# Kernel tuning notes

Measured on AMD Instinct MI355X. Metric: run time of the kernel, lower is better.

The kernel has to match this reference:

```python
import jax, jax.numpy as jnp
import numpy as np

B, T, I, H, L = 32768, 30, 4, 64, 32


def _lstm_layer(x, Wih, Whh, bih, bhh):
    """PyTorch-semantics single-layer LSTM, batch_first. Returns (outputs [B,T,H], h_T [B,H])."""
    # Precompute input contribution for all timesteps: [B, T, 4H]
    xg = jnp.einsum('bti,gi->btg', x, Wih) + bih + bhh
    Hh = Whh.shape[1]
    h0 = jnp.zeros((x.shape[0], Hh), x.dtype)

    def step(carry, xg_t):
        h, c = carry
        g = xg_t + h @ Whh.T  # [B, 4H]
        i, f, gg, o = jnp.split(g, 4, axis=-1)  # PyTorch gate order i,f,g,o
        c = jax.nn.sigmoid(f) * c + jax.nn.sigmoid(i) * jnp.tanh(gg)
        h = jax.nn.sigmoid(o) * jnp.tanh(c)
        return (h, c), h

    (hT, _), hs = jax.lax.scan(step, (h0, h0), jnp.swapaxes(xg, 0, 1))
    return jnp.swapaxes(hs, 0, 1), hT


def setup_inputs() -> dict:
    key = jax.random.key(0)
    ks = jax.random.split(key, 20)
    s = 0.1  # weight scale for numerical stability
    inp = {
        'x': jax.random.normal(ks[0], (B, T, I), jnp.float32),
        'enc1_Wih': s * jax.random.normal(ks[1], (4 * H, I), jnp.float32),
        'enc1_Whh': s * jax.random.normal(ks[2], (4 * H, H), jnp.float32),
        'enc1_bih': s * jax.random.normal(ks[3], (4 * H,), jnp.float32),
        'enc1_bhh': s * jax.random.normal(ks[4], (4 * H,), jnp.float32),
        'enc2_Wih': s * jax.random.normal(ks[5], (4 * L, H), jnp.float32),
        'enc2_Whh': s * jax.random.normal(ks[6], (4 * L, L), jnp.float32),
        'enc2_bih': s * jax.random.normal(ks[7], (4 * L,), jnp.float32),
        'enc2_bhh': s * jax.random.normal(ks[8], (4 * L,), jnp.float32),
        'dec1_Wih': s * jax.random.normal(ks[9], (4 * H, L), jnp.float32),
        'dec1_Whh': s * jax.random.normal(ks[10], (4 * H, H), jnp.float32),
        'dec1_bih': s * jax.random.normal(ks[11], (4 * H,), jnp.float32),
        'dec1_bhh': s * jax.random.normal(ks[12], (4 * H,), jnp.float32),
        'dec2_Wih': s * jax.random.normal(ks[13], (4 * I, H), jnp.float32),
        'dec2_Whh': s * jax.random.normal(ks[14], (4 * I, I), jnp.float32),
        'dec2_bih': s * jax.random.normal(ks[15], (4 * I,), jnp.float32),
        'dec2_bhh': s * jax.random.normal(ks[16], (4 * I,), jnp.float32),
    }
    return inp


def reference(x, enc1_Wih, enc1_Whh, enc1_bih, enc1_bhh,
              enc2_Wih, enc2_Whh, enc2_bih, enc2_bhh,
              dec1_Wih, dec1_Whh, dec1_bih, dec1_bhh,
              dec2_Wih, dec2_Whh, dec2_bih, dec2_bhh):
    seq_len = x.shape[1]
    out, _ = _lstm_layer(x, enc1_Wih, enc1_Whh, enc1_bih, enc1_bhh)
    out, h = _lstm_layer(out, enc2_Wih, enc2_Whh, enc2_bih, enc2_bhh)
    latent = jnp.repeat(h[:, None, :], seq_len, axis=1)  # [B, T, L]
    out, _ = _lstm_layer(latent, dec1_Wih, dec1_Whh, dec1_bih, dec1_bhh)
    out, _ = _lstm_layer(out, dec2_Wih, dec2_Whh, dec2_bih, dec2_bhh)
    return out
```

## Files before the change

### kernel.cpp

```cpp
#include <hip/hip_runtime.h>
#include <stdint.h>


typedef unsigned short u16;
typedef unsigned int u32;
typedef __attribute__((ext_vector_type(8))) short bf16x8;
typedef __attribute__((ext_vector_type(4))) float f32x4;
typedef __attribute__((ext_vector_type(16))) float f32x16;
typedef __attribute__((ext_vector_type(4))) u32 u32x4;
typedef __attribute__((ext_vector_type(2))) u32 u32x2;

#define BATCH 32768
#define TT 30
#define IN 4
#define WAVES 12
#define BLOCKT (WAVES * 64)
#define MBC 32
#define NCL 4
#define BPB (NCL * MBC)

#define LOG2E 1.4426950408889634f
#define LOG2E2 2.8853900817779268f

#define O_WHH1 0
#define O_FOLD 8192
#define O_WIH2 10240
#define O_WHH2 14336
#define O_WHH3 0
#define O_WIH3 8192
#define O_WIH4 12288
#define O_W4HHF 12800
#define O_B2F 16384
#define O_B3F 16512
#define O_B4F 16768
#define O_BUFS 16784
#define PBUF 1664
#define SMEM_WORDS (O_BUFS + NCL * PBUF)
#define SMEM_BYTES (SMEM_WORDS * 4)

#define WB() __builtin_amdgcn_wave_barrier()
#define MFMA32(a, b, c) __builtin_amdgcn_mfma_f32_32x32x16_bf16((a), (b), (c), 0, 0, 0)
#define MFMA16(a, b, c) __builtin_amdgcn_mfma_f32_16x16x32_bf16((a), (b), (c), 0, 0, 0)

__device__ __forceinline__ u16 f2bf(float f) {
    u32 u = __float_as_uint(f);
    u += 0x7fffu + ((u >> 16) & 1u);
    return (u16)(u >> 16);
}
__device__ __forceinline__ float bf2f(u16 v) { return __uint_as_float(((u32)v) << 16); }

__device__ __forceinline__ u32 cvtpk2(float a, float b) {
    u32 d;
    asm("v_cvt_pk_bf16_f32 %0, %1, %2" : "=v"(d) : "v"(a), "v"(b));
    return d;
}

__device__ __forceinline__ float unitH(float yi, float yf, float yg, float yo, float& c) {
    const float ei = __builtin_amdgcn_exp2f(-yi);
    const float ef = __builtin_amdgcn_exp2f(-yf);
    const float eg = __builtin_amdgcn_exp2f(yg);
    const float eo = __builtin_amdgcn_exp2f(-yo);
    const float Z = (1.f + ei) * (1.f + eg);
    const float X = 1.f + ef;
    const float num = fmaf(eg - 1.f, X, c * Z);
    c = num * __builtin_amdgcn_rcpf(X * Z);
    const float ec = __builtin_amdgcn_exp2f(c * LOG2E2);
    return (ec - 1.f) * __builtin_amdgcn_rcpf((1.f + eo) * (1.f + ec));
}

template <int KT16, int GS>
__device__ __forceinline__ void stage32(u16* dst, const float* src, int N, int tid) {
    const int K = KT16 * 16;
    const int total = N * K;
    for (int idx = tid; idx < total; idx += BLOCKT) {
        const int j = idx & 7;
        const int l = (idx >> 3) & 63;
        const int pr = idx >> 9;
        const int kt = pr % KT16;
        const int nt = pr / KT16;
        const int n = nt * 32 + (l & 31);
        const int k = kt * 16 + ((l >> 5) << 3) + j;
        const float s = (((n >> GS) & 3) == 2) ? LOG2E2 : LOG2E;
        dst[idx] = f2bf(src[n * K + k] * s);
    }
}

template <int KT, int GS>
__device__ __forceinline__ void stage16(u16* dst, const float* src, int N, int tid) {
    const int K = KT * 32;
    const int total = N * K;
    for (int idx = tid; idx < total; idx += BLOCKT) {
        const int j = idx & 7;
        const int l = (idx >> 3) & 63;
        const int pr = idx >> 9;
        const int kt = pr & (KT - 1);
        const int nt = pr / KT;
        const int n = (nt << 4) | (l & 15);
        const int k = (kt << 5) + ((l >> 4) << 3) + j;
        const float s = (((n >> GS) & 3) == 2) ? LOG2E2 : LOG2E;
        dst[idx] = f2bf(src[n * K + k] * s);
    }
}

#define LD8(P, IDX) (*reinterpret_cast<const bf16x8*>((P) + ((IDX) * 64 + lane) * 8))

#define BINIT(DST, BP, RB)                                                               \
    _Pragma("unroll") for (int p_ = 0; p_ < 4; ++p_) {                                   \
        const f32x4 b_ = *reinterpret_cast<const f32x4*>((BP) + (RB) + p_ * 8 + 4 * hi); \
        (DST)[4 * p_ + 0] = b_[0]; (DST)[4 * p_ + 1] = b_[1];                            \
        (DST)[4 * p_ + 2] = b_[2]; (DST)[4 * p_ + 3] = b_[3];                            \
    }

#define CELL16(AI, AF, AG, AO, CST, IMG, BKT)                                                        \
    _Pragma("unroll") for (int p_ = 0; p_ < 4; ++p_) {                                               \
        const float h0_ = unitH((AI)[4*p_+0], (AF)[4*p_+0], (AG)[4*p_+0], (AO)[4*p_+0], (CST)[4*p_+0]); \
        const float h1_ = unitH((AI)[4*p_+1], (AF)[4*p_+1], (AG)[4*p_+1], (AO)[4*p_+1], (CST)[4*p_+1]); \
        const float h2_ = unitH((AI)[4*p_+2], (AF)[4*p_+2], (AG)[4*p_+2], (AO)[4*p_+2], (CST)[4*p_+2]); \
        const float h3_ = unitH((AI)[4*p_+3], (AF)[4*p_+3], (AG)[4*p_+3], (AO)[4*p_+3], (CST)[4*p_+3]); \
        u32x2 wv_;                                                                                   \
        wv_.x = cvtpk2(h0_, h1_);                                                                    \
        wv_.y = cvtpk2(h2_, h3_);                                                                    \
        *reinterpret_cast<u32x2*>((IMG) + (((BKT) + (p_ >> 1)) * 64 + (p_ & 1) * 32 + c31) * 8 + 4 * hi) = wv_; \
    }

#define E1G(DST, G) {                                                  \
        f32x16 a_ = MFMA32(foldr[G], xB, z16);                         \
        a_ = MFMA32(LD8(Whh1p, (2 * (G) + role) * 4 + 0), h1B0, a_);   \
        a_ = MFMA32(LD8(Whh1p, (2 * (G) + role) * 4 + 1), h1B1, a_);   \
        a_ = MFMA32(LD8(Whh1p, (2 * (G) + role) * 4 + 2), h1B2, a_);   \
        a_ = MFMA32(LD8(Whh1p, (2 * (G) + role) * 4 + 3), h1B3, a_);   \
        DST = a_; }

#define E2G(DST, G) {                                                  \
        f32x16 a_; BINIT(a_, b2f, (G) * 32)                            \
        a_ = MFMA32(LD8(Wih2p, (G) * 4 + 0), h1B0, a_);                \
        a_ = MFMA32(LD8(Wih2p, (G) * 4 + 1), h1B1, a_);                \
        a_ = MFMA32(LD8(Wih2p, (G) * 4 + 2), h1B2, a_);                \
        a_ = MFMA32(LD8(Wih2p, (G) * 4 + 3), h1B3, a_);                \
        a_ = MFMA32(LD8(Whh2p, (G) * 2 + 0), h2B0, a_);                \
        a_ = MFMA32(LD8(Whh2p, (G) * 2 + 1), h2B1, a_);                \
        DST = a_; }

#define D1G(DST, G) {                                                  \
        f32x16 a_; BINIT(a_, b3f, (2 * (G) + role) * 32)               \
        a_ = MFMA32(LD8(Wih3p, (2 * (G) + role) * 2 + 0), latB0, a_);  \
        a_ = MFMA32(LD8(Wih3p, (2 * (G) + role) * 2 + 1), latB1, a_);  \
        a_ = MFMA32(LD8(Whh3p, (2 * (G) + role) * 4 + 0), h3B0, a_);   \
        a_ = MFMA32(LD8(Whh3p, (2 * (G) + role) * 4 + 1), h3B1, a_);   \
        a_ = MFMA32(LD8(Whh3p, (2 * (G) + role) * 4 + 2), h3B2, a_);   \
        a_ = MFMA32(LD8(Whh3p, (2 * (G) + role) * 4 + 3), h3B3, a_);   \
        DST = a_; }
#define D1G0(DST, G) {                                                 \
        f32x16 a_; BINIT(a_, b3f, (2 * (G) + role) * 32)               \
        a_ = MFMA32(LD8(Wih3p, (2 * (G) + role) * 2 + 0), latB0, a_);  \
        a_ = MFMA32(LD8(Wih3p, (2 * (G) + role) * 2 + 1), latB1, a_);  \
        DST = a_; }

#define D2ADDR(M, BH) ((((2 * (M) + (quad >> 1)) * 64) + (quad & 1) * 32 + (BH) * 16 + col16) * 8)

#define DEC2BODY(T) {                                                                   \
        f32x4 a0 = b4v, a1 = b4v;                                                       \
        _Pragma("unroll") for (int r_ = 0; r_ < 4; ++r_) {                              \
            float s0 = a0[r_], s1 = a1[r_];                                             \
            s0 = fmaf(w4r[r_].x, hv0.x, s0); s0 = fmaf(w4r[r_].y, hv0.y, s0);           \
            s0 = fmaf(w4r[r_].z, hv0.z, s0); s0 = fmaf(w4r[r_].w, hv0.w, s0);           \
            s1 = fmaf(w4r[r_].x, hv1.x, s1); s1 = fmaf(w4r[r_].y, hv1.y, s1);           \
            s1 = fmaf(w4r[r_].z, hv1.z, s1); s1 = fmaf(w4r[r_].w, hv1.w, s1);           \
            a0[r_] = s0; a1[r_] = s1;                                                   \
        }                                                                               \
        a0 = MFMA16(w4a0, dB00, a0); a0 = MFMA16(w4a1, dB10, a0);                       \
        a1 = MFMA16(w4a0, dB01, a1); a1 = MFMA16(w4a1, dB11, a1);                       \
        WB();                                                                           \
        *reinterpret_cast<f32x4*>(gbuf + col16 * 16 + quad * 4) = a0;                   \
        *reinterpret_cast<f32x4*>(gbuf + (16 + col16) * 16 + quad * 4) = a1;            \
        WB();                                                                           \
        {                                                                               \
            const int u4_ = lane & 3, mb_ = lane >> 2;                                  \
            const float h0_ = unitH(gbuf[mb_ * 16 + u4_], gbuf[mb_ * 16 + 4 + u4_],     \
                                    gbuf[mb_ * 16 + 8 + u4_], gbuf[mb_ * 16 + 12 + u4_], c4a); \
            out[((size_t)(b0w + mb_) * TT + (T)) * IN + u4_] = h0_;                     \
            bufH4[mb_ * 4 + u4_] = h0_;                                                 \
            const int b1_ = 16 + mb_;                                                   \
            const float h1_ = unitH(gbuf[b1_ * 16 + u4_], gbuf[b1_ * 16 + 4 + u4_],     \
                                    gbuf[b1_ * 16 + 8 + u4_], gbuf[b1_ * 16 + 12 + u4_], c4b); \
            out[((size_t)(b0w + b1_) * TT + (T)) * IN + u4_] = h1_;                     \
            bufH4[b1_ * 4 + u4_] = h1_;                                                 \
        }                                                                               \
        WB(); }

__global__ __launch_bounds__(BLOCKT)
void lstm_ae(
    const float* __restrict__ x,
    const float* __restrict__ w1ih, const float* __restrict__ w1hh,
    const float* __restrict__ b1i, const float* __restrict__ b1h,
    const float* __restrict__ w2ih, const float* __restrict__ w2hh,
    const float* __restrict__ b2i, const float* __restrict__ b2h,
    const float* __restrict__ w3ih, const float* __restrict__ w3hh,
    const float* __restrict__ b3i, const float* __restrict__ b3h,
    const float* __restrict__ w4ih, const float* __restrict__ w4hh,
    const float* __restrict__ b4i, const float* __restrict__ b4h,
    float* __restrict__ out) {
    extern __shared__ float smem[];
    float* W = smem;

    const int tid = threadIdx.x;
    const int wave = tid >> 6, lane = tid & 63;
    const int cl = wave / 3, role = wave % 3;
    const int c31 = lane & 31, hi = lane >> 5;
    const int col16 = lane & 15, quad = lane >> 4;

    float* pb = smem + O_BUFS + cl * PBUF;
    u16* h1img = (u16*)pb;
    u16* h2img = (u16*)(pb + 1024);
    float* gbuf = pb + 1024;
    float* bufH4 = pb + 1536;

    const int b0w = blockIdx.x * BPB + cl * MBC;

    stage32<4, 6>((u16*)(W + O_WHH1), w1hh, 256, tid);
    stage32<4, 5>((u16*)(W + O_WIH2), w2ih, 128, tid);
    stage32<2, 5>((u16*)(W + O_WHH2), w2hh, 128, tid);
    {
        u16* F = (u16*)(W + O_FOLD);
        for (int idx = tid; idx < 4096; idx += BLOCKT) {
            const int j = idx & 7;
            const int l = (idx >> 3) & 63;
            const int nt = idx >> 9;
            const int m = nt * 32 + (l & 31);
            const int hif = l >> 5;
            const float sc = ((m >> 6) == 2) ? LOG2E2 : LOG2E;
            u16 v = 0;
            if (!hif) {
                v = f2bf(w1ih[m * 4 + (j & 3)] * sc);
            } else if (j < 4) {
                const float w = w1ih[m * 4 + j] * sc;
                v = f2bf(w - bf2f(f2bf(w)));
            } else if (j == 4) {
                v = f2bf((b1i[m] + b1h[m]) * sc);
            } else if (j == 5) {
                const float b = (b1i[m] + b1h[m]) * sc;
                v = f2bf(b - bf2f(f2bf(b)));
            }
            F[idx] = v;
        }
    }
    float* b2f = W + O_B2F;
    float* b3f = W + O_B3F;
    float* b4f = W + O_B4F;
    for (int i = tid; i < 128; i += BLOCKT)
        b2f[i] = (b2i[i] + b2h[i]) * (((i >> 5) == 2) ? LOG2E2 : LOG2E);
    for (int i = tid; i < 256; i += BLOCKT)
        b3f[i] = (b3i[i] + b3h[i]) * (((i >> 6) == 2) ? LOG2E2 : LOG2E);
    for (int i = tid; i < 16; i += BLOCKT)
        b4f[i] = (b4i[i] + b4h[i]) * (((i >> 2) == 2) ? LOG2E2 : LOG2E);
    if (role == 2) {
        u32* z = (u32*)h2img;
        for (int i = lane; i < 512; i += 64) z[i] = 0u;
    }
    __syncthreads();

    const u16* Whh1p = (const u16*)(W + O_WHH1);
    const u16* Wih2p = (const u16*)(W + O_WIH2);
    const u16* Whh2p = (const u16*)(W + O_WHH2);
    const u16* FOLDp = (const u16*)(W + O_FOLD);

    const f32x16 z16 = {0.f, 0.f, 0.f, 0.f, 0.f, 0.f, 0.f, 0.f,
                        0.f, 0.f, 0.f, 0.f, 0.f, 0.f, 0.f, 0.f};
    float cst[16];
#pragma unroll
    for (int r = 0; r < 16; ++r) cst[r] = 0.f;

    bf16x8 foldr[4] = {};
    if (role < 2) {
#pragma unroll
        for (int g = 0; g < 4; ++g) foldr[g] = LD8(FOLDp, 2 * g + role);
    }

    float4 xcur = {0.f, 0.f, 0.f, 0.f};
    if (role < 2)
        xcur = *reinterpret_cast<const float4*>(x + ((size_t)(b0w + c31) * TT + 0) * IN);

    auto buildX = [&](const float4 xc) -> bf16x8 {
        const u32 h01 = cvtpk2(xc.x, xc.y);
        const u32 h23 = cvtpk2(xc.z, xc.w);
        const float r0 = xc.x - __uint_as_float(h01 << 16);
        const float r1 = xc.y - __uint_as_float(h01 & 0xffff0000u);
        const float r2 = xc.z - __uint_as_float(h23 << 16);
        const float r3 = xc.w - __uint_as_float(h23 & 0xffff0000u);
        const u32 l01 = cvtpk2(r0, r1);
        const u32 l23 = cvtpk2(r2, r3);
        u32x4 v;
        v.x = h01;
        v.y = h23;
        v.z = hi ? 0x3F803F80u : l01;
        v.w = hi ? 0u : l23;
        return __builtin_bit_cast(bf16x8, v);
    };

    if (role < 2) {
        const bf16x8 xB = buildX(xcur);
        xcur = *reinterpret_cast<const float4*>(x + ((size_t)(b0w + c31) * TT + 1) * IN);
        f32x16 aI = MFMA32(foldr[0], xB, z16);
        f32x16 aF = MFMA32(foldr[1], xB, z16);
        f32x16 aG = MFMA32(foldr[2], xB, z16);
        f32x16 aO = MFMA32(foldr[3], xB, z16);
        CELL16(aI, aF, aG, aO, cst, h1img, 2 * role)
    }
    __syncthreads();

    for (int t = 0; t < TT - 1; ++t) {
        const bf16x8 h1B0 = *reinterpret_cast<const bf16x8*>(h1img + (0 * 64 + lane) * 8);
        const bf16x8 h1B1 = *reinterpret_cast<const bf16x8*>(h1img + (1 * 64 + lane) * 8);
        const bf16x8 h1B2 = *reinterpret_cast<const bf16x8*>(h1img + (2 * 64 + lane) * 8);
        const bf16x8 h1B3 = *reinterpret_cast<const bf16x8*>(h1img + (3 * 64 + lane) * 8);
        bf16x8 h2B0 = {}, h2B1 = {};
        if (role == 2) {
            h2B0 = *reinterpret_cast<const bf16x8*>(h2img + (0 * 64 + lane) * 8);
            h2B1 = *reinterpret_cast<const bf16x8*>(h2img + (1 * 64 + lane) * 8);
        }
        __syncthreads();
        if (role == 2) {
            f32x16 aI, aF, aG, aO;
            E2G(aI, 0) E2G(aF, 1) E2G(aG, 2) E2G(aO, 3)
            CELL16(aI, aF, aG, aO, cst, h2img, 0)
        } else {
            const bf16x8 xB = buildX(xcur);
            const int tn = (t + 2 < TT) ? t + 2 : TT - 1;
            xcur = *reinterpret_cast<const float4*>(x + ((size_t)(b0w + c31) * TT + tn) * IN);
            f32x16 aI, aF, aG, aO;
            E1G(aI, 0) E1G(aF, 1) E1G(aG, 2) E1G(aO, 3)
            CELL16(aI, aF, aG, aO, cst, h1img, 2 * role)
        }
        __syncthreads();
    }
    if (role == 2) {
        const bf16x8 h1B0 = *reinterpret_cast<const bf16x8*>(h1img + (0 * 64 + lane) * 8);
        const bf16x8 h1B1 = *reinterpret_cast<const bf16x8*>(h1img + (1 * 64 + lane) * 8);
        const bf16x8 h1B2 = *reinterpret_cast<const bf16x8*>(h1img + (2 * 64 + lane) * 8);
        const bf16x8 h1B3 = *reinterpret_cast<const bf16x8*>(h1img + (3 * 64 + lane) * 8);
        const bf16x8 h2B0 = *reinterpret_cast<const bf16x8*>(h2img + (0 * 64 + lane) * 8);
        const bf16x8 h2B1 = *reinterpret_cast<const bf16x8*>(h2img + (1 * 64 + lane) * 8);
        f32x16 aI, aF, aG, aO;
        E2G(aI, 0) E2G(aF, 1) E2G(aG, 2) E2G(aO, 3)
        CELL16(aI, aF, aG, aO, cst, h2img, 0)
    }
    __syncthreads();

    stage32<4, 6>((u16*)(W + O_WHH3), w3hh, 256, tid);
    stage32<2, 6>((u16*)(W + O_WIH3), w3ih, 256, tid);
    stage16<2, 2>((u16*)(W + O_WIH4), w4ih, 16, tid);
    for (int i = tid; i < 64; i += BLOCKT)
        W[O_W4HHF + i] = w4hh[i] * ((((i >> 4) & 3) == 2) ? LOG2E2 : LOG2E);

    float c4a = 0.f, c4b = 0.f;
    bf16x8 latB0 = {}, latB1 = {};
    if (role < 2) {
        latB0 = *reinterpret_cast<const bf16x8*>(h2img + (0 * 64 + lane) * 8);
        latB1 = *reinterpret_cast<const bf16x8*>(h2img + (1 * 64 + lane) * 8);
    } else {
        for (int i = lane; i < 128; i += 64) bufH4[i] = 0.f;
    }
#pragma unroll
    for (int r = 0; r < 16; ++r) cst[r] = 0.f;
    __syncthreads();

    const u16* Whh3p = (const u16*)(W + O_WHH3);
    const u16* Wih3p = (const u16*)(W + O_WIH3);
    const u16* Wih4p = (const u16*)(W + O_WIH4);
    const float* W4hhF = W + O_W4HHF;
    bf16x8 w4a0 = {}, w4a1 = {};
    f32x4 b4v = {0.f, 0.f, 0.f, 0.f};
    float4 w4r[4] = {};
    if (role == 2) {
        w4a0 = LD8(Wih4p, 0);
        w4a1 = LD8(Wih4p, 1);
        b4v = *reinterpret_cast<const f32x4*>(b4f + quad * 4);
#pragma unroll
        for (int r = 0; r < 4; ++r)
            w4r[r] = *reinterpret_cast<const float4*>(W4hhF + (quad * 4 + r) * 4);
    }

    if (role < 2) {
        f32x16 aI, aF, aG, aO;
        D1G0(aI, 0) D1G0(aF, 1) D1G0(aG, 2) D1G0(aO, 3)
        CELL16(aI, aF, aG, aO, cst, h1img, 2 * role)
    }
    __syncthreads();

    for (int t = 0; t < TT - 1; ++t) {
        bf16x8 h3B0 = {}, h3B1 = {}, h3B2 = {}, h3B3 = {};
        bf16x8 dB00 = {}, dB10 = {}, dB01 = {}, dB11 = {};
        float4 hv0 = {0.f, 0.f, 0.f, 0.f}, hv1 = {0.f, 0.f, 0.f, 0.f};
        if (role < 2) {
            h3B0 = *reinterpret_cast<const bf16x8*>(h1img + (0 * 64 + lane) * 8);
            h3B1 = *reinterpret_cast<const bf16x8*>(h1img + (1 * 64 + lane) * 8);
            h3B2 = *reinterpret_cast<const bf16x8*>(h1img + (2 * 64 + lane) * 8);
            h3B3 = *reinterpret_cast<const bf16x8*>(h1img + (3 * 64 + lane) * 8);
        } else {
            dB00 = *reinterpret_cast<const bf16x8*>(h1img + D2ADDR(0, 0));
            dB10 = *reinterpret_cast<const bf16x8*>(h1img + D2ADDR(1, 0));
            dB01 = *reinterpret_cast<const bf16x8*>(h1img + D2ADDR(0, 1));
            dB11 = *reinterpret_cast<const bf16x8*>(h1img + D2ADDR(1, 1));
            hv0 = *reinterpret_cast<const float4*>(bufH4 + col16 * 4);
            hv1 = *reinterpret_cast<const float4*>(bufH4 + (16 + col16) * 4);
        }
        __syncthreads();
        if (role == 2) {
            DEC2BODY(t)
        } else {
            f32x16 aI, aF, aG, aO;
            D1G(aI, 0) D1G(aF, 1) D1G(aG, 2) D1G(aO, 3)
            CELL16(aI, aF, aG, aO, cst, h1img, 2 * role)
        }
        __syncthreads();
    }
    if (role == 2) {
        const bf16x8 dB00 = *reinterpret_cast<const bf16x8*>(h1img + D2ADDR(0, 0));
        const bf16x8 dB10 = *reinterpret_cast<const bf16x8*>(h1img + D2ADDR(1, 0));
        const bf16x8 dB01 = *reinterpret_cast<const bf16x8*>(h1img + D2ADDR(0, 1));
        const bf16x8 dB11 = *reinterpret_cast<const bf16x8*>(h1img + D2ADDR(1, 1));
        const float4 hv0 = *reinterpret_cast<const float4*>(bufH4 + col16 * 4);
        const float4 hv1 = *reinterpret_cast<const float4*>(bufH4 + (16 + col16) * 4);
        DEC2BODY(TT - 1)
    }
}

extern "C" void kernel_launch(void* const* d_in, const int* in_sizes, int n_in,
                              void* d_out, int out_size, void* d_ws, size_t ws_size,
                              hipStream_t stream) {
    (void)in_sizes; (void)n_in; (void)d_ws; (void)ws_size; (void)out_size;
    hipFuncSetAttribute(reinterpret_cast<const void*>(lstm_ae),
                        hipFuncAttributeMaxDynamicSharedMemorySize, SMEM_BYTES);
    const float* xi = (const float*)d_in[0];
    const float* w1ih = (const float*)d_in[1];
    const float* w1hh = (const float*)d_in[2];
    const float* b1i = (const float*)d_in[3];
    const float* b1h = (const float*)d_in[4];
    const float* w2ih = (const float*)d_in[5];
    const float* w2hh = (const float*)d_in[6];
    const float* b2i = (const float*)d_in[7];
    const float* b2h = (const float*)d_in[8];
    const float* w3ih = (const float*)d_in[9];
    const float* w3hh = (const float*)d_in[10];
    const float* b3i = (const float*)d_in[11];
    const float* b3h = (const float*)d_in[12];
    const float* w4ih = (const float*)d_in[13];
    const float* w4hh = (const float*)d_in[14];
    const float* b4i = (const float*)d_in[15];
    const float* b4h = (const float*)d_in[16];
    float* out = (float*)d_out;

    lstm_ae<<<dim3(BATCH / BPB), dim3(BLOCKT), SMEM_BYTES, stream>>>(
        xi, w1ih, w1hh, b1i, b1h, w2ih, w2hh, b2i, b2h,
        w3ih, w3hh, b3i, b3h, w4ih, w4hh, b4i, b4h, out);
}
```

Before: 286.1 us.

## Double-buffer hidden-state images to drop one barrier per timestep and hoist constant gate terms

Hidden-state images for layers 1/2 and 3 are now ping-ponged between two LDS buffers indexed by timestep parity. Each step can then read the previous image and write the next one without an intermediate __syncthreads, halving the barriers per step. The loop-invariant latent input contribution to decoder layer 1 and the encoder-2 bias are precomputed once into registers, and launch bounds ask for 3 blocks per CU. The cost is more LDS per cluster (PBUF nearly doubles) and extra accumulator registers, which may limit occupancy.

```diff
diff --git a/kernel.cpp b/kernel.cpp
--- a/kernel.cpp
+++ b/kernel.cpp
@@ -34,7 +34,7 @@
 #define O_B3F 16512
 #define O_B4F 16768
 #define O_BUFS 16784
-#define PBUF 1664
+#define PBUF 3200
 #define SMEM_WORDS (O_BUFS + NCL * PBUF)
 #define SMEM_BYTES (SMEM_WORDS * 4)
 
@@ -132,7 +132,7 @@
         DST = a_; }
 
 #define E2G(DST, G) {                                                  \
-        f32x16 a_; BINIT(a_, b2f, (G) * 32)                            \
+        f32x16 a_ = b2r[G];                                            \
         a_ = MFMA32(LD8(Wih2p, (G) * 4 + 0), h1B0, a_);                \
         a_ = MFMA32(LD8(Wih2p, (G) * 4 + 1), h1B1, a_);                \
         a_ = MFMA32(LD8(Wih2p, (G) * 4 + 2), h1B2, a_);                \
@@ -142,23 +142,22 @@
         DST = a_; }
 
 #define D1G(DST, G) {                                                  \
-        f32x16 a_; BINIT(a_, b3f, (2 * (G) + role) * 32)               \
-        a_ = MFMA32(LD8(Wih3p, (2 * (G) + role) * 2 + 0), latB0, a_);  \
-        a_ = MFMA32(LD8(Wih3p, (2 * (G) + role) * 2 + 1), latB1, a_);  \
+        f32x16 a_ = latA[G];                                           \
         a_ = MFMA32(LD8(Whh3p, (2 * (G) + role) * 4 + 0), h3B0, a_);   \
         a_ = MFMA32(LD8(Whh3p, (2 * (G) + role) * 4 + 1), h3B1, a_);   \
         a_ = MFMA32(LD8(Whh3p, (2 * (G) + role) * 4 + 2), h3B2, a_);   \
         a_ = MFMA32(LD8(Whh3p, (2 * (G) + role) * 4 + 3), h3B3, a_);   \
         DST = a_; }
-#define D1G0(DST, G) {                                                 \
-        f32x16 a_; BINIT(a_, b3f, (2 * (G) + role) * 32)               \
-        a_ = MFMA32(LD8(Wih3p, (2 * (G) + role) * 2 + 0), latB0, a_);  \
-        a_ = MFMA32(LD8(Wih3p, (2 * (G) + role) * 2 + 1), latB1, a_);  \
-        DST = a_; }
 
 #define D2ADDR(M, BH) ((((2 * (M) + (quad >> 1)) * 64) + (quad & 1) * 32 + (BH) * 16 + col16) * 8)
 
-#define DEC2BODY(T) {                                                                   \
+#define DEC2BODY(T, H3R) {                                                              \
+        const bf16x8 dB00 = *reinterpret_cast<const bf16x8*>((H3R) + D2ADDR(0, 0));     \
+        const bf16x8 dB10 = *reinterpret_cast<const bf16x8*>((H3R) + D2ADDR(1, 0));     \
+        const bf16x8 dB01 = *reinterpret_cast<const bf16x8*>((H3R) + D2ADDR(0, 1));     \
+        const bf16x8 dB11 = *reinterpret_cast<const bf16x8*>((H3R) + D2ADDR(1, 1));     \
+        const float4 hv0 = *reinterpret_cast<const float4*>(bufH4 + col16 * 4);         \
+        const float4 hv1 = *reinterpret_cast<const float4*>(bufH4 + (16 + col16) * 4);  \
         f32x4 a0 = b4v, a1 = b4v;                                                       \
         _Pragma("unroll") for (int r_ = 0; r_ < 4; ++r_) {                              \
             float s0 = a0[r_], s1 = a1[r_];                                             \
@@ -188,7 +187,7 @@
         }                                                                               \
         WB(); }
 
-__global__ __launch_bounds__(BLOCKT)
+__global__ __launch_bounds__(BLOCKT, 3)
 void lstm_ae(
     const float* __restrict__ x,
     const float* __restrict__ w1ih, const float* __restrict__ w1hh,
@@ -210,10 +209,10 @@
     const int col16 = lane & 15, quad = lane >> 4;
 
     float* pb = smem + O_BUFS + cl * PBUF;
-    u16* h1img = (u16*)pb;
-    u16* h2img = (u16*)(pb + 1024);
-    float* gbuf = pb + 1024;
-    float* bufH4 = pb + 1536;
+    u16* h1d = (u16*)pb;
+    u16* h2d = (u16*)(pb + 2048);
+    float* gbuf = pb + 2048;
+    float* bufH4 = pb + 3072;
 
     const int b0w = blockIdx.x * BPB + cl * MBC;
 
@@ -254,8 +253,8 @@
     for (int i = tid; i < 16; i += BLOCKT)
         b4f[i] = (b4i[i] + b4h[i]) * (((i >> 2) == 2) ? LOG2E2 : LOG2E);
     if (role == 2) {
-        u32* z = (u32*)h2img;
-        for (int i = lane; i < 512; i += 64) z[i] = 0u;
+        u32* z = (u32*)pb;
+        for (int i = lane; i < 512; i += 64) z[2048 + i] = 0u;
     }
     __syncthreads();
 
@@ -271,9 +270,13 @@
     for (int r = 0; r < 16; ++r) cst[r] = 0.f;
 
     bf16x8 foldr[4] = {};
+    f32x16 b2r[4];
     if (role < 2) {
 #pragma unroll
         for (int g = 0; g < 4; ++g) foldr[g] = LD8(FOLDp, 2 * g + role);
+    } else {
+#pragma unroll
+        for (int g = 0; g < 4; ++g) { BINIT(b2r[g], b2f, g * 32) }
     }
 
     float4 xcur = {0.f, 0.f, 0.f, 0.f};
@@ -304,45 +307,52 @@
         f32x16 aF = MFMA32(foldr[1], xB, z16);
         f32x16 aG = MFMA32(foldr[2], xB, z16);
         f32x16 aO = MFMA32(foldr[3], xB, z16);
-        CELL16(aI, aF, aG, aO, cst, h1img, 2 * role)
+        CELL16(aI, aF, aG, aO, cst, h1d, 2 * role)
     }
     __syncthreads();
 
     for (int t = 0; t < TT - 1; ++t) {
-        const bf16x8 h1B0 = *reinterpret_cast<const bf16x8*>(h1img + (0 * 64 + lane) * 8);
-        const bf16x8 h1B1 = *reinterpret_cast<const bf16x8*>(h1img + (1 * 64 + lane) * 8);
-        const bf16x8 h1B2 = *reinterpret_cast<const bf16x8*>(h1img + (2 * 64 + lane) * 8);
-        const bf16x8 h1B3 = *reinterpret_cast<const bf16x8*>(h1img + (3 * 64 + lane) * 8);
-        bf16x8 h2B0 = {}, h2B1 = {};
+        const u16* h1r = h1d + ((t & 1) << 11);
+        u16* h1w = h1d + (((t + 1) & 1) << 11);
+        const u16* h2r = h2d + ((t & 1) << 10);
+        u16* h2w = h2d + (((t + 1) & 1) << 10);
         if (role == 2) {
-            h2B0 = *reinterpret_cast<const bf16x8*>(h2img + (0 * 64 + lane) * 8);
-            h2B1 = *reinterpret_cast<const bf16x8*>(h2img + (1 * 64 + lane) * 8);
-        }
-        __syncthreads();
-        if (role == 2) {
+            const bf16x8 h1B0 = *reinterpret_cast<const bf16x8*>(h1r + (0 * 64 + lane) * 8);
+            const bf16x8 h1B1 = *reinterpret_cast<const bf16x8*>(h1r + (1 * 64 + lane) * 8);
+            const bf16x8 h1B2 = *reinterpret_cast<const bf16x8*>(h1r + (2 * 64 + lane) * 8);
+            const bf16x8 h1B3 = *reinterpret_cast<const bf16x8*>(h1r + (3 * 64 + lane) * 8);
+            const bf16x8 h2B0 = *reinterpret_cast<const bf16x8*>(h2r + (0 * 64 + lane) * 8);
+            const bf16x8 h2B1 = *reinterpret_cast<const bf16x8*>(h2r + (1 * 64 + lane) * 8);
             f32x16 aI, aF, aG, aO;
             E2G(aI, 0) E2G(aF, 1) E2G(aG, 2) E2G(aO, 3)
-            CELL16(aI, aF, aG, aO, cst, h2img, 0)
+            CELL16(aI, aF, aG, aO, cst, h2w, 0)
         } else {
+            const bf16x8 h1B0 = *reinterpret_cast<const bf16x8*>(h1r + (0 * 64 + lane) * 8);
+            const bf16x8 h1B1 = *reinterpret_cast<const bf16x8*>(h1r + (1 * 64 + lane) * 8);
+            const bf16x8 h1B2 = *reinterpret_cast<const bf16x8*>(h1r + (2 * 64 + lane) * 8);
+            const bf16x8 h1B3 = *reinterpret_cast<const bf16x8*>(h1r + (3 * 64 + lane) * 8);
             const bf16x8 xB = buildX(xcur);
             const int tn = (t + 2 < TT) ? t + 2 : TT - 1;
             xcur = *reinterpret_cast<const float4*>(x + ((size_t)(b0w + c31) * TT + tn) * IN);
             f32x16 aI, aF, aG, aO;
             E1G(aI, 0) E1G(aF, 1) E1G(aG, 2) E1G(aO, 3)
-            CELL16(aI, aF, aG, aO, cst, h1img, 2 * role)
+            CELL16(aI, aF, aG, aO, cst, h1w, 2 * role)
         }
         __syncthreads();
     }
     if (role == 2) {
-        const bf16x8 h1B0 = *reinterpret_cast<const bf16x8*>(h1img + (0 * 64 + lane) * 8);
-        const bf16x8 h1B1 = *reinterpret_cast<const bf16x8*>(h1img + (1 * 64 + lane) * 8);
-        const bf16x8 h1B2 = *reinterpret_cast<const bf16x8*>(h1img + (2 * 64 + lane) * 8);
-        const bf16x8 h1B3 = *reinterpret_cast<const bf16x8*>(h1img + (3 * 64 + lane) * 8);
-        const bf16x8 h2B0 = *reinterpret_cast<const bf16x8*>(h2img + (0 * 64 + lane) * 8);
-        const bf16x8 h2B1 = *reinterpret_cast<const bf16x8*>(h2img + (1 * 64 + lane) * 8);
+        const u16* h1r = h1d + (((TT - 1) & 1) << 11);
+        const u16* h2r = h2d + (((TT - 1) & 1) << 10);
+        u16* h2w = h2d;
+        const bf16x8 h1B0 = *reinterpret_cast<const bf16x8*>(h1r + (0 * 64 + lane) * 8);
+        const bf16x8 h1B1 = *reinterpret_cast<const bf16x8*>(h1r + (1 * 64 + lane) * 8);
+        const bf16x8 h1B2 = *reinterpret_cast<const bf16x8*>(h1r + (2 * 64 + lane) * 8);
+        const bf16x8 h1B3 = *reinterpret_cast<const bf16x8*>(h1r + (3 * 64 + lane) * 8);
+        const bf16x8 h2B0 = *reinterpret_cast<const bf16x8*>(h2r + (0 * 64 + lane) * 8);
+        const bf16x8 h2B1 = *reinterpret_cast<const bf16x8*>(h2r + (1 * 64 + lane) * 8);
         f32x16 aI, aF, aG, aO;
         E2G(aI, 0) E2G(aF, 1) E2G(aG, 2) E2G(aO, 3)
-        CELL16(aI, aF, aG, aO, cst, h2img, 0)
+        CELL16(aI, aF, aG, aO, cst, h2w, 0)
     }
     __syncthreads();
 
@@ -355,8 +365,8 @@
     float c4a = 0.f, c4b = 0.f;
     bf16x8 latB0 = {}, latB1 = {};
     if (role < 2) {
-        latB0 = *reinterpret_cast<const bf16x8*>(h2img + (0 * 64 + lane) * 8);
-        latB1 = *reinterpret_cast<const bf16x8*>(h2img + (1 * 64 + lane) * 8);
+        latB0 = *reinterpret_cast<const bf16x8*>(h2d + (0 * 64 + lane) * 8);
+        latB1 = *reinterpret_cast<const bf16x8*>(h2d + (1 * 64 + lane) * 8);
     } else {
         for (int i = lane; i < 128; i += 64) bufH4[i] = 0.f;
     }
@@ -371,7 +381,17 @@
     bf16x8 w4a0 = {}, w4a1 = {};
     f32x4 b4v = {0.f, 0.f, 0.f, 0.f};
     float4 w4r[4] = {};
-    if (role == 2) {
+    f32x16 latA[4];
+    if (role < 2) {
+#pragma unroll
+        for (int g = 0; g < 4; ++g) {
+            f32x16 a;
+            BINIT(a, b3f, (2 * g + role) * 32)
+            a = MFMA32(LD8(Wih3p, (2 * g + role) * 2 + 0), latB0, a);
+            a = MFMA32(LD8(Wih3p, (2 * g + role) * 2 + 1), latB1, a);
+            latA[g] = a;
+        }
+    } else {
         w4a0 = LD8(Wih4p, 0);
         w4a1 = LD8(Wih4p, 1);
         b4v = *reinterpret_cast<const f32x4*>(b4f + quad * 4);
@@ -381,47 +401,29 @@
     }
 
     if (role < 2) {
-        f32x16 aI, aF, aG, aO;
-        D1G0(aI, 0) D1G0(aF, 1) D1G0(aG, 2) D1G0(aO, 3)
-        CELL16(aI, aF, aG, aO, cst, h1img, 2 * role)
+        CELL16(latA[0], latA[1], latA[2], latA[3], cst, h1d, 2 * role)
     }
     __syncthreads();
 
     for (int t = 0; t < TT - 1; ++t) {
-        bf16x8 h3B0 = {}, h3B1 = {}, h3B2 = {}, h3B3 = {};
-        bf16x8 dB00 = {}, dB10 = {}, dB01 = {}, dB11 = {};
-        float4 hv0 = {0.f, 0.f, 0.f, 0.f}, hv1 = {0.f, 0.f, 0.f, 0.f};
-        if (role < 2) {
-            h3B0 = *reinterpret_cast<const bf16x8*>(h1img + (0 * 64 + lane) * 8);
-            h3B1 = *reinterpret_cast<const bf16x8*>(h1img + (1 * 64 + lane) * 8);
-            h3B2 = *reinterpret_cast<const bf16x8*>(h1img + (2 * 64 + lane) * 8);
-            h3B3 = *reinterpret_cast<const bf16x8*>(h1img + (3 * 64 + lane) * 8);
+        const u16* h3r = h1d + ((t & 1) << 11);
+        u16* h3w = h1d + (((t + 1) & 1) << 11);
+        if (role == 2) {
+            DEC2BODY(t, h3r)
         } else {
-            dB00 = *reinterpret_cast<const bf16x8*>(h1img + D2ADDR(0, 0));
-            dB10 = *reinterpret_cast<const bf16x8*>(h1img + D2ADDR(1, 0));
-            dB01 = *reinterpret_cast<const bf16x8*>(h1img + D2ADDR(0, 1));
-            dB11 = *reinterpret_cast<const bf16x8*>(h1img + D2ADDR(1, 1));
-            hv0 = *reinterpret_cast<const float4*>(bufH4 + col16 * 4);
-            hv1 = *reinterpret_cast<const float4*>(bufH4 + (16 + col16) * 4);
+            const bf16x8 h3B0 = *reinterpret_cast<const bf16x8*>(h3r + (0 * 64 + lane) * 8);
+            const bf16x8 h3B1 = *reinterpret_cast<const bf16x8*>(h3r + (1 * 64 + lane) * 8);
+            const bf16x8 h3B2 = *reinterpret_cast<const bf16x8*>(h3r + (2 * 64 + lane) * 8);
+            const bf16x8 h3B3 = *reinterpret_cast<const bf16x8*>(h3r + (3 * 64 + lane) * 8);
+            f32x16 aI, aF, aG, aO;
+            D1G(aI, 0) D1G(aF, 1) D1G(aG, 2) D1G(aO, 3)
+            CELL16(aI, aF, aG, aO, cst, h3w, 2 * role)
         }
         __syncthreads();
-        if (role == 2) {
-            DEC2BODY(t)
-        } else {
-            f32x16 aI, aF, aG, aO;
-            D1G(aI, 0) D1G(aF, 1) D1G(aG, 2) D1G(aO, 3)
-            CELL16(aI, aF, aG, aO, cst, h1img, 2 * role)
-        }
-        __syncthreads();
     }
     if (role == 2) {
-        const bf16x8 dB00 = *reinterpret_cast<const bf16x8*>(h1img + D2ADDR(0, 0));
-        const bf16x8 dB10 = *reinterpret_cast<const bf16x8*>(h1img + D2ADDR(1, 0));
-        const bf16x8 dB01 = *reinterpret_cast<const bf16x8*>(h1img + D2ADDR(0, 1));
-        const bf16x8 dB11 = *reinterpret_cast<const bf16x8*>(h1img + D2ADDR(1, 1));
-        const float4 hv0 = *reinterpret_cast<const float4*>(bufH4 + col16 * 4);
-        const float4 hv1 = *reinterpret_cast<const float4*>(bufH4 + (16 + col16) * 4);
-        DEC2BODY(TT - 1)
+        const u16* h3r = h1d + (((TT - 1) & 1) << 11);
+        DEC2BODY(TT - 1, h3r)
     }
 }
 
```

Measured after the change: 464.1 us. 1.62x slower.
